# Performance work log

Hardware: AMD Instinct MI355X
Metric: run time of the kernel (lower is better)

## Reference

```python
import jax, jax.numpy as jnp
import numpy as np

B, S, D = 2, 1024, 2048
H, KV, HD = 16, 4, 128
GROUPS = H // KV
THETA = 10000.0


def act_quant(xr, xi):
    # per-token 8-bit absmax quantization over last dim, joint scale for re/im, STE
    amax = jnp.maximum(jnp.max(jnp.abs(xr), -1, keepdims=True),
                       jnp.max(jnp.abs(xi), -1, keepdims=True))
    s = 127.0 / jnp.maximum(amax, 1e-5)
    qr = jnp.clip(jnp.round(xr * s), -128, 127) / s
    qi = jnp.clip(jnp.round(xi * s), -128, 127) / s
    return xr + jax.lax.stop_gradient(qr - xr), xi + jax.lax.stop_gradient(qi - xi)


def weight_quant(wr, wi):
    # Fairy+-i direction quantization: each weight -> scale * d, d in {+1,-1,+i,-i}; STE
    mag = jnp.mean(jnp.sqrt(wr * wr + wi * wi))
    use_re = jnp.abs(wr) >= jnp.abs(wi)
    qr = jnp.where(use_re, jnp.sign(wr) * mag, 0.0)
    qi = jnp.where(use_re, 0.0, jnp.sign(wi) * mag)
    return wr + jax.lax.stop_gradient(qr - wr), wi + jax.lax.stop_gradient(qi - wi)


def complex_linear(xr, xi, wr, wi):
    xr, xi = act_quant(xr, xi)
    wr, wi = weight_quant(wr, wi)
    o_re = xr @ wr - xi @ wi
    o_im = xr @ wi + xi @ wr
    return o_re, o_im


def rotate_half(x):
    h = x.shape[-1] // 2
    return jnp.concatenate([-x[..., h:], x[..., :h]], axis=-1)


def rope_tables():
    inv_freq = 1.0 / (THETA ** (jnp.arange(0, HD, 2, dtype=jnp.float32) / HD))
    pos = jnp.arange(S, dtype=jnp.float32)
    freqs = pos[:, None] * inv_freq[None, :]          # [S, HD/2]
    emb = jnp.concatenate([freqs, freqs], axis=-1)    # [S, HD]
    return jnp.cos(emb)[None, None], jnp.sin(emb)[None, None]  # [1,1,S,HD]


def _heads(x, n):
    # [B,S,n*HD] -> [B,n,S,HD]
    return x.reshape(B, S, n, HD).transpose(0, 2, 1, 3)


def _attn(hidden_real, hidden_imag, wq_re, wq_im, wk_re, wk_im,
          wv_re, wv_im, wo_re, wo_im):
    q_re, q_im = complex_linear(hidden_real, hidden_imag, wq_re, wq_im)
    k_re, k_im = complex_linear(hidden_real, hidden_imag, wk_re, wk_im)
    v_re, v_im = complex_linear(hidden_real, hidden_imag, wv_re, wv_im)

    q_re, q_im = _heads(q_re, H), _heads(q_im, H)      # [B,H,S,HD]
    k_re, k_im = _heads(k_re, KV), _heads(k_im, KV)    # [B,KV,S,HD]
    v_re, v_im = _heads(v_re, KV), _heads(v_im, KV)

    cos, sin = rope_tables()
    # RoPE applied only to real components of q and k
    q_re = q_re * cos + rotate_half(q_re) * sin
    k_re = k_re * cos + rotate_half(k_re) * sin

    # GQA repeat
    k_re = jnp.repeat(k_re, GROUPS, axis=1)
    k_im = jnp.repeat(k_im, GROUPS, axis=1)
    v_re = jnp.repeat(v_re, GROUPS, axis=1)
    v_im = jnp.repeat(v_im, GROUPS, axis=1)

    # real scores = Re(q . conj(k)) = q_re.k_re + q_im.k_im
    scores = (jnp.einsum('bhqd,bhkd->bhqk', q_re, k_re) +
              jnp.einsum('bhqd,bhkd->bhqk', q_im, k_im)) / jnp.sqrt(jnp.float32(HD))
    causal = jnp.tril(jnp.ones((S, S), dtype=bool))
    scores = jnp.where(causal[None, None], scores, jnp.finfo(scores.dtype).min)
    attn = jax.nn.softmax(scores, axis=-1)

    o_re = jnp.einsum('bhqk,bhkd->bhqd', attn, v_re)
    o_im = jnp.einsum('bhqk,bhkd->bhqd', attn, v_im)
    o_re = o_re.transpose(0, 2, 1, 3).reshape(B, S, H * HD)
    o_im = o_im.transpose(0, 2, 1, 3).reshape(B, S, H * HD)

    out_re, out_im = complex_linear(o_re, o_im, wo_re, wo_im)
    return jnp.stack([out_re, out_im])  # [2,B,S,D]


def setup_inputs() -> dict:
    key = jax.random.key(0)
    ks = jax.random.split(key, 12)
    w = lambda k, shp: jax.random.normal(k, shp, dtype=jnp.float32) * 0.02
    return {
        'hidden_real': jax.random.normal(ks[0], (B, S, D), dtype=jnp.float32),
        'hidden_imag': jax.random.normal(ks[1], (B, S, D), dtype=jnp.float32),
        'wq_re': w(ks[2], (D, H * HD)), 'wq_im': w(ks[3], (D, H * HD)),
        'wk_re': w(ks[4], (D, KV * HD)), 'wk_im': w(ks[5], (D, KV * HD)),
        'wv_re': w(ks[6], (D, KV * HD)), 'wv_im': w(ks[7], (D, KV * HD)),
        'wo_re': w(ks[8], (H * HD, D)), 'wo_im': w(ks[9], (H * HD, D)),
    }


def reference(hidden_real, hidden_imag, wq_re, wq_im, wk_re, wk_im,
              wv_re, wv_im, wo_re, wo_im):
    return _attn(hidden_real, hidden_imag, wq_re, wq_im, wk_re, wk_im,
                 wv_re, wv_im, wo_re, wo_im)
```

## Files before the change

### kernel.cpp

```cpp
#include <hip/hip_runtime.h>
#include <stdint.h>

#define B_   2
#define S_   1024
#define D_   2048
#define H_   16
#define KV_  4
#define HD_  128
#define NTOK (B_ * S_)
#define QD   (H_ * HD_)
#define KD   (KV_ * HD_)

using i32x4  = __attribute__((ext_vector_type(4)))  int;
using i32x16 = __attribute__((ext_vector_type(16))) int;
using f32x4  = __attribute__((ext_vector_type(4)))  float;
using bf16x8 = __attribute__((ext_vector_type(8)))  short;

#define LN1E4_OVER_64 0.14391156831212725f

__device__ __forceinline__ float bf2f(uint16_t u) { return __uint_as_float((uint32_t)u << 16); }
__device__ __forceinline__ uint16_t f2bf(float f) {
    uint32_t u = __float_as_uint(f);
    return (uint16_t)((u + 0x7FFFu + ((u >> 16) & 1u)) >> 16);
}

__global__ __launch_bounds__(256)
void act_quant_i8_kernel(const float* __restrict__ xr, const float* __restrict__ xi,
                         int8_t* __restrict__ qr, int8_t* __restrict__ qi,
                         float* __restrict__ invs)
{
    const int tok = blockIdx.x, t = threadIdx.x;
    const float* pr = xr + (size_t)tok * 2048 + t * 8;
    const float* pi = xi + (size_t)tok * 2048 + t * 8;
    float4 r0 = *(const float4*)pr, r1 = *(const float4*)(pr + 4);
    float4 i0 = *(const float4*)pi, i1 = *(const float4*)(pi + 4);
    float am = fmaxf(fmaxf(fmaxf(fabsf(r0.x), fabsf(r0.y)), fmaxf(fabsf(r0.z), fabsf(r0.w))),
                     fmaxf(fmaxf(fabsf(r1.x), fabsf(r1.y)), fmaxf(fabsf(r1.z), fabsf(r1.w))));
    am = fmaxf(am, fmaxf(fmaxf(fmaxf(fabsf(i0.x), fabsf(i0.y)), fmaxf(fabsf(i0.z), fabsf(i0.w))),
                         fmaxf(fmaxf(fabsf(i1.x), fabsf(i1.y)), fmaxf(fabsf(i1.z), fabsf(i1.w)))));
    __shared__ float red[256];
    red[t] = am;
    __syncthreads();
    for (int st = 128; st > 0; st >>= 1) {
        if (t < st) red[t] = fmaxf(red[t], red[t + st]);
        __syncthreads();
    }
    const float s = 127.0f / fmaxf(red[0], 1e-5f);
    if (t == 0) invs[tok] = 1.0f / s;
#define Q8(x) ((uint32_t)(uint8_t)(int8_t)(int)fminf(fmaxf(rintf((x) * s), -128.f), 127.f))
    uint32_t a0 = Q8(r0.x) | (Q8(r0.y) << 8) | (Q8(r0.z) << 16) | (Q8(r0.w) << 24);
    uint32_t a1 = Q8(r1.x) | (Q8(r1.y) << 8) | (Q8(r1.z) << 16) | (Q8(r1.w) << 24);
    uint32_t b0 = Q8(i0.x) | (Q8(i0.y) << 8) | (Q8(i0.z) << 16) | (Q8(i0.w) << 24);
    uint32_t b1 = Q8(i1.x) | (Q8(i1.y) << 8) | (Q8(i1.z) << 16) | (Q8(i1.w) << 24);
#undef Q8
    *(uint32_t*)(qr + (size_t)tok * 2048 + t * 8)     = a0;
    *(uint32_t*)(qr + (size_t)tok * 2048 + t * 8 + 4) = a1;
    *(uint32_t*)(qi + (size_t)tok * 2048 + t * 8)     = b0;
    *(uint32_t*)(qi + (size_t)tok * 2048 + t * 8 + 4) = b1;
}

__global__ __launch_bounds__(256)
void decode_kernel(const float* __restrict__ wr, const float* __restrict__ wi,
                   int N, int8_t* __restrict__ psr, int8_t* __restrict__ psi,
                   int8_t* __restrict__ pnsi, int n_off, float* __restrict__ mag_out)
{
    __shared__ alignas(16) int8_t tr[3][64][80];
    __shared__ float red[256];
    const int n0 = blockIdx.x * 64, k0 = blockIdx.y * 64;
    float msum = 0.f;
    for (int idx = threadIdx.x; idx < 4096; idx += 256) {
        int j = idx & 63, i = idx >> 6;
        size_t g = (size_t)(k0 + i) * N + n0 + j;
        float a = wr[g], b = wi[g];
        msum += sqrtf(a * a + b * b);
        int8_t sr, si;
        if (fabsf(a) >= fabsf(b)) {
            sr = (a > 0.f) ? 1 : ((a < 0.f) ? -1 : 0);
            si = 0;
        } else {
            sr = 0;
            si = (b > 0.f) ? 1 : ((b < 0.f) ? -1 : 0);
        }
        tr[0][j][i] = sr;
        tr[1][j][i] = si;
        tr[2][j][i] = (int8_t)(-si);
    }
    red[threadIdx.x] = msum;
    __syncthreads();
    for (int st = 128; st > 0; st >>= 1) {
        if (threadIdx.x < st) red[threadIdx.x] += red[threadIdx.x + st];
        __syncthreads();
    }
    if (threadIdx.x == 0) atomicAdd(mag_out, red[0]);
    int8_t* planes[3] = { psr, psi, pnsi };
    for (int idx = threadIdx.x; idx < 768; idx += 256) {
        int p = idx >> 8, rem = idx & 255, n = rem >> 2, c = rem & 3;
        int4 v = *(const int4*)&tr[p][n][c * 16];
        *(int4*)(planes[p] + (size_t)(n_off + n0 + n) * 2048 + k0 + c * 16) = v;
    }
}

__device__ __forceinline__ void async_copy16(const void* g, void* l) {
    __builtin_amdgcn_global_load_lds((const __attribute__((address_space(1))) void*)g,
                                     (__attribute__((address_space(3))) void*)l, 16, 0, 0);
}

template <int MODE>
__global__ __launch_bounds__(256)
void gemm_i8_kernel(const int8_t* __restrict__ axr, const int8_t* __restrict__ axi,
                    const int8_t* __restrict__ bsr, const int8_t* __restrict__ bsi,
                    const int8_t* __restrict__ bnsi,
                    int Nout, const float* __restrict__ invs,
                    const float* __restrict__ mag_sums,
                    float magc0, float magc1, float magc2,
                    float* o_re, float* o_im,
                    uint16_t* kbr, uint16_t* kbi, uint16_t* vbr, uint16_t* vbi)
{
    __shared__ alignas(16) int8_t smem[2][5 * 8192];
    const int tid = threadIdx.x;
    const int wav = tid >> 6, lane = tid & 63;
    const int tileM = blockIdx.y * 128, tileN = blockIdx.x * 128;
    const int wm = wav & 1, wn = wav >> 1;
    const int K = 2048;

    const int8_t* gplane[5] = { axr, axi, bsr, bsi, bnsi };
    const int     rbase[5]  = { tileM, tileM, tileN, tileN, tileN };

    i32x16 acc_re[2][2] = {};
    i32x16 acc_im[2][2] = {};

    auto issue_tile = [&](int k0, int buf) {
#pragma unroll
        for (int i = 0; i < 10; ++i) {
            int q = wav + 4 * i;
            int pl = q >> 3, seg = q & 7;
            int c = seg >> 1, m0 = (seg & 1) << 6;
            const int8_t* g = gplane[pl] + (size_t)(rbase[pl] + m0 + lane) * K + k0 + c * 16;
            int8_t* l = &smem[buf][pl * 8192 + (c * 128 + m0) * 16];
            async_copy16(g, l);
        }
    };

    issue_tile(0, 0);
    issue_tile(64, 1);

    for (int k = 0; k < 32; ++k) {
        if (k == 31) { asm volatile("s_waitcnt vmcnt(0)" ::: "memory"); }
        else         { asm volatile("s_waitcnt vmcnt(10)" ::: "memory"); }
        asm volatile("s_barrier" ::: "memory");
        const int8_t* sb = smem[k & 1];
#pragma unroll
        for (int s = 0; s < 2; ++s) {
            const int cc = 2 * s + (lane >> 5);
            const int rA = wm * 64 + (lane & 31);
            const int rB = wn * 64 + (lane & 31);
            i32x4 fxr[2], fxi[2], fsr[2], fsi[2], fns[2];
#pragma unroll
            for (int mb = 0; mb < 2; ++mb) {
                int off = (cc * 128 + rA + mb * 32) * 16;
                fxr[mb] = *(const i32x4*)&sb[0 * 8192 + off];
                fxi[mb] = *(const i32x4*)&sb[1 * 8192 + off];
            }
#pragma unroll
            for (int nb = 0; nb < 2; ++nb) {
                int off = (cc * 128 + rB + nb * 32) * 16;
                fsr[nb] = *(const i32x4*)&sb[2 * 8192 + off];
                fsi[nb] = *(const i32x4*)&sb[3 * 8192 + off];
                fns[nb] = *(const i32x4*)&sb[4 * 8192 + off];
            }
#pragma unroll
            for (int mb = 0; mb < 2; ++mb)
#pragma unroll
                for (int nb = 0; nb < 2; ++nb) {
                    acc_re[mb][nb] = __builtin_amdgcn_mfma_i32_32x32x32_i8(fxr[mb], fsr[nb], acc_re[mb][nb], 0, 0, 0);
                    acc_re[mb][nb] = __builtin_amdgcn_mfma_i32_32x32x32_i8(fxi[mb], fns[nb], acc_re[mb][nb], 0, 0, 0);
                    acc_im[mb][nb] = __builtin_amdgcn_mfma_i32_32x32x32_i8(fxr[mb], fsi[nb], acc_im[mb][nb], 0, 0, 0);
                    acc_im[mb][nb] = __builtin_amdgcn_mfma_i32_32x32x32_i8(fxi[mb], fsr[nb], acc_im[mb][nb], 0, 0, 0);
                }
        }
        asm volatile("s_barrier" ::: "memory");
        if (k + 2 < 32) issue_tile((k + 2) * 64, k & 1);
    }

    const int ln31 = lane & 31, lq = lane >> 5;
#pragma unroll
    for (int mb = 0; mb < 2; ++mb) {
#pragma unroll
        for (int nb = 0; nb < 2; ++nb) {
            const int gn = tileN + wn * 64 + nb * 32 + ln31;
            float mag;
            if (MODE == 0)
                mag = (gn < 2048) ? mag_sums[0] * magc0
                    : (gn < 2560) ? mag_sums[1] * magc1
                                  : mag_sums[2] * magc2;
            else
                mag = mag_sums[0] * magc0;
#pragma unroll
            for (int r = 0; r < 16; ++r) {
                const int row = (r & 3) + 8 * (r >> 2) + 4 * lq;
                const int gm = tileM + wm * 64 + mb * 32 + row;
                const float sc = mag * invs[gm];
                const float re = (float)acc_re[mb][nb][r] * sc;
                const float im = (float)acc_im[mb][nb][r] * sc;
                if (MODE == 1) {
                    o_re[(size_t)gm * Nout + gn] = re;
                    o_im[(size_t)gm * Nout + gn] = im;
                } else {
                    const int s = gm & (S_ - 1), bb = gm >> 10;
                    if (gn < 2048) {
                        o_re[(size_t)gm * 2048 + gn] = re;
                        o_im[(size_t)gm * 2048 + gn] = im;
                    } else if (gn < 2560) {
                        int c = gn - 2048, kvh = c >> 7, d = c & 127;
                        size_t off = ((size_t)(bb * KV_ + kvh) * S_ + s) * 128 + d;
                        kbr[off] = f2bf(re);
                        kbi[off] = f2bf(im);
                    } else {
                        int c = gn - 2560, kvh = c >> 7, d = c & 127;
                        size_t off = ((size_t)(bb * KV_ + kvh) * S_ + s) * 128 + d;
                        vbr[off] = f2bf(re);
                        vbi[off] = f2bf(im);
                    }
                }
            }
        }
    }
}

__global__ __launch_bounds__(256)
void rope_q_kernel(const float* __restrict__ q_re, const float* __restrict__ q_im,
                   uint16_t* __restrict__ qb_re, uint16_t* __restrict__ qb_im)
{
    int gidx = blockIdx.x * 256 + threadIdx.x;
    int j = gidx & 15, h = (gidx >> 4) & 15, tok = gidx >> 8;
    int s = tok & (S_ - 1), b = tok >> 10;
    int d0 = j * 4;
    size_t ib = (size_t)tok * 2048 + h * 128;
    float4 r0 = *(const float4*)&q_re[ib + d0];
    float4 r1 = *(const float4*)&q_re[ib + d0 + 64];
    float4 i0 = *(const float4*)&q_im[ib + d0];
    float4 i1 = *(const float4*)&q_im[ib + d0 + 64];
    float ro0[4], ro1[4];
    float rv0[4] = { r0.x, r0.y, r0.z, r0.w };
    float rv1[4] = { r1.x, r1.y, r1.z, r1.w };
#pragma unroll
    for (int t = 0; t < 4; ++t) {
        float f = __expf(-(float)(d0 + t) * LN1E4_OVER_64);
        float sn, c;
        __sincosf((float)s * f, &sn, &c);
        ro0[t] = rv0[t] * c - rv1[t] * sn;
        ro1[t] = rv1[t] * c + rv0[t] * sn;
    }
    size_t ob = ((size_t)(b * H_ + h) * S_ + s) * 128;
    ushort4 w;
    w = (ushort4){ f2bf(ro0[0]), f2bf(ro0[1]), f2bf(ro0[2]), f2bf(ro0[3]) };
    *(ushort4*)&qb_re[ob + d0] = w;
    w = (ushort4){ f2bf(ro1[0]), f2bf(ro1[1]), f2bf(ro1[2]), f2bf(ro1[3]) };
    *(ushort4*)&qb_re[ob + d0 + 64] = w;
    w = (ushort4){ f2bf(i0.x), f2bf(i0.y), f2bf(i0.z), f2bf(i0.w) };
    *(ushort4*)&qb_im[ob + d0] = w;
    w = (ushort4){ f2bf(i1.x), f2bf(i1.y), f2bf(i1.z), f2bf(i1.w) };
    *(ushort4*)&qb_im[ob + d0 + 64] = w;
}

__global__ __launch_bounds__(256)
void rope_k_kernel(uint16_t* __restrict__ kb_re)
{
    int gidx = blockIdx.x * 256 + threadIdx.x;
    int j = gidx & 15, kvh = (gidx >> 4) & 3;
    int rest = gidx >> 6;
    int s = rest & (S_ - 1), b = rest >> 10;
    int d0 = j * 4;
    size_t base = ((size_t)(b * KV_ + kvh) * S_ + s) * 128;
    ushort4 u0 = *(const ushort4*)&kb_re[base + d0];
    ushort4 u1 = *(const ushort4*)&kb_re[base + d0 + 64];
    float rv0[4] = { bf2f(u0.x), bf2f(u0.y), bf2f(u0.z), bf2f(u0.w) };
    float rv1[4] = { bf2f(u1.x), bf2f(u1.y), bf2f(u1.z), bf2f(u1.w) };
    float ro0[4], ro1[4];
#pragma unroll
    for (int t = 0; t < 4; ++t) {
        float f = __expf(-(float)(d0 + t) * LN1E4_OVER_64);
        float sn, c;
        __sincosf((float)s * f, &sn, &c);
        ro0[t] = rv0[t] * c - rv1[t] * sn;
        ro1[t] = rv1[t] * c + rv0[t] * sn;
    }
    *(ushort4*)&kb_re[base + d0]      = (ushort4){ f2bf(ro0[0]), f2bf(ro0[1]), f2bf(ro0[2]), f2bf(ro0[3]) };
    *(ushort4*)&kb_re[base + d0 + 64] = (ushort4){ f2bf(ro1[0]), f2bf(ro1[1]), f2bf(ro1[2]), f2bf(ro1[3]) };
}

__global__ __launch_bounds__(256)
void vtrans_kernel(const uint16_t* __restrict__ vbr, const uint16_t* __restrict__ vbi,
                   uint16_t* __restrict__ vtr, uint16_t* __restrict__ vti)
{
    __shared__ uint16_t t[32][36];
    const int pl = blockIdx.z & 1, bk = blockIdx.z >> 1;
    const int s0 = blockIdx.x * 32, d0 = blockIdx.y * 32;
    const uint16_t* src = (pl ? vbi : vbr) + ((size_t)bk * S_) * 128;
    uint16_t*       dst = (pl ? vti : vtr) + ((size_t)bk * 128) * S_;
    const int r = threadIdx.x >> 3, c = (threadIdx.x & 7) * 4;
    *(ushort4*)&t[r][c] = *(const ushort4*)&src[(size_t)(s0 + r) * 128 + d0 + c];
    __syncthreads();
    ushort4 o = (ushort4){ t[c][r], t[c + 1][r], t[c + 2][r], t[c + 3][r] };
    *(ushort4*)&dst[(size_t)(d0 + r) * S_ + s0 + c] = o;
}

__global__ __launch_bounds__(256)
void attn_mfma_kernel(const uint16_t* __restrict__ qb_re, const uint16_t* __restrict__ qb_im,
                      const uint16_t* __restrict__ kb_re, const uint16_t* __restrict__ kb_im,
                      const uint16_t* __restrict__ vt_re, const uint16_t* __restrict__ vt_im,
                      float* __restrict__ o_re, float* __restrict__ o_im)
{
    __shared__ alignas(16) uint16_t sk[2][32][136];
    __shared__ alignas(16) uint16_t sv[2][128][40];
    __shared__ alignas(16) uint16_t sp[4][16][40];

    const int tid = threadIdx.x;
    const int w = tid >> 6, lane = tid & 63;
    const int r16 = lane & 15, q4 = lane >> 4;
    const int qt = gridDim.x - 1 - blockIdx.x;
    const int h = blockIdx.y, b = blockIdx.z;
    const int kvh = h >> 2;
    const int q0 = qt * 64, qw0 = q0 + w * 16;

    bf16x8 qfr[4], qfi[4];
    {
        const size_t qbase = ((size_t)(b * H_ + h) * S_ + qw0 + r16) * 128;
#pragma unroll
        for (int ks = 0; ks < 4; ++ks) {
            const int col = ks * 32 + q4 * 8;
            qfr[ks] = *(const bf16x8*)&qb_re[qbase + col];
            qfi[ks] = *(const bf16x8*)&qb_im[qbase + col];
        }
    }

    f32x4 oa[2][8] = {};
    float m_r[4] = { -3e38f, -3e38f, -3e38f, -3e38f };
    float l_r[4] = { 0.f, 0.f, 0.f, 0.f };

    const size_t kgbase0 = (size_t)(b * KV_ + kvh) * S_ * 128;
    const size_t vgbase0 = (size_t)(b * KV_ + kvh) * 128 * (size_t)S_;

    for (int c0 = 0; c0 < q0 + 64; c0 += 32) {
        for (int idx = tid; idx < 1024; idx += 256) {
            int pl = idx >> 9, c = idx & 511, r = c >> 4, ch = c & 15;
            const uint16_t* src = (pl ? kb_im : kb_re) + kgbase0 + (size_t)(c0 + r) * 128 + ch * 8;
            *(uint4*)&sk[pl][r][ch * 8] = *(const uint4*)src;
        }
        for (int idx = tid; idx < 1024; idx += 256) {
            int pl = idx >> 9, c = idx & 511, d = c >> 2, ch = c & 3;
            const uint16_t* src = (pl ? vt_im : vt_re) + vgbase0 + (size_t)d * S_ + c0 + ch * 8;
            *(uint4*)&sv[pl][d][ch * 8] = *(const uint4*)src;
        }
        __syncthreads();

        if (c0 <= qw0 + 15) {
            f32x4 sc[2] = {};
#pragma unroll
            for (int cblk = 0; cblk < 2; ++cblk) {
                const int krow = cblk * 16 + r16;
#pragma unroll
                for (int ks = 0; ks < 4; ++ks) {
                    const int kcol = ks * 32 + q4 * 8;
                    bf16x8 kr = *(const bf16x8*)&sk[0][krow][kcol];
                    bf16x8 ki = *(const bf16x8*)&sk[1][krow][kcol];
                    sc[cblk] = __builtin_amdgcn_mfma_f32_16x16x32_bf16(qfr[ks], kr, sc[cblk], 0, 0, 0);
                    sc[cblk] = __builtin_amdgcn_mfma_f32_16x16x32_bf16(qfi[ks], ki, sc[cblk], 0, 0, 0);
                }
            }
#pragma unroll
            for (int cblk = 0; cblk < 2; ++cblk)
#pragma unroll
                for (int reg = 0; reg < 4; ++reg) {
                    float sval = sc[cblk][reg] * 0.08838834764831845f;
                    const int rowg = qw0 + q4 * 4 + reg;
                    const int colg = c0 + cblk * 16 + r16;
                    if (colg > rowg) sval = -3e38f;
                    sc[cblk][reg] = sval;
                }
            float al[4];
#pragma unroll
            for (int reg = 0; reg < 4; ++reg) {
                float mx = fmaxf(sc[0][reg], sc[1][reg]);
#pragma unroll
                for (int msk = 1; msk < 16; msk <<= 1) mx = fmaxf(mx, __shfl_xor(mx, msk));
                const float mn = fmaxf(m_r[reg], mx);
                al[reg] = __expf(m_r[reg] - mn);
                const float p0 = __expf(sc[0][reg] - mn);
                const float p1 = __expf(sc[1][reg] - mn);
                sc[0][reg] = p0; sc[1][reg] = p1;
                float rs = p0 + p1;
#pragma unroll
                for (int msk = 1; msk < 16; msk <<= 1) rs += __shfl_xor(rs, msk);
                l_r[reg] = l_r[reg] * al[reg] + rs;
                m_r[reg] = mn;
            }
#pragma unroll
            for (int cblk = 0; cblk < 2; ++cblk)
#pragma unroll
                for (int reg = 0; reg < 4; ++reg)
                    sp[w][q4 * 4 + reg][cblk * 16 + r16] = f2bf(sc[cblk][reg]);
#pragma unroll
            for (int dblk = 0; dblk < 8; ++dblk)
#pragma unroll
                for (int reg = 0; reg < 4; ++reg) {
                    oa[0][dblk][reg] *= al[reg];
                    oa[1][dblk][reg] *= al[reg];
                }
            bf16x8 pf = *(const bf16x8*)&sp[w][r16][q4 * 8];
#pragma unroll
            for (int dblk = 0; dblk < 8; ++dblk) {
                const int vrow = dblk * 16 + r16;
                bf16x8 vr = *(const bf16x8*)&sv[0][vrow][q4 * 8];
                bf16x8 vi = *(const bf16x8*)&sv[1][vrow][q4 * 8];
                oa[0][dblk] = __builtin_amdgcn_mfma_f32_16x16x32_bf16(pf, vr, oa[0][dblk], 0, 0, 0);
                oa[1][dblk] = __builtin_amdgcn_mfma_f32_16x16x32_bf16(pf, vi, oa[1][dblk], 0, 0, 0);
            }
        }
        __syncthreads();
    }

    float inv[4];
#pragma unroll
    for (int reg = 0; reg < 4; ++reg) inv[reg] = 1.f / l_r[reg];
#pragma unroll
    for (int dblk = 0; dblk < 8; ++dblk) {
        const int col = h * 128 + dblk * 16 + r16;
#pragma unroll
        for (int reg = 0; reg < 4; ++reg) {
            const size_t tok = (size_t)b * S_ + qw0 + q4 * 4 + reg;
            o_re[tok * 2048 + col] = oa[0][dblk][reg] * inv[reg];
            o_im[tok * 2048 + col] = oa[1][dblk][reg] * inv[reg];
        }
    }
}

extern "C" void kernel_launch(void* const* d_in, const int* in_sizes, int n_in,
                              void* d_out, int out_size, void* d_ws, size_t ws_size,
                              hipStream_t stream)
{
    const float* hr    = (const float*)d_in[0];
    const float* hi    = (const float*)d_in[1];
    const float* wq_re = (const float*)d_in[2];
    const float* wq_im = (const float*)d_in[3];
    const float* wk_re = (const float*)d_in[4];
    const float* wk_im = (const float*)d_in[5];
    const float* wv_re = (const float*)d_in[6];
    const float* wv_im = (const float*)d_in[7];
    const float* wo_re = (const float*)d_in[8];
    const float* wo_im = (const float*)d_in[9];
    float* out = (float*)d_out;
    char*  base = (char*)d_ws;

    const size_t MB4  = (size_t)2048 * 2048;
    const size_t QKVP = (size_t)3072 * 2048;
    const size_t KVE  = (size_t)B_ * KV_ * S_ * 128;

    float*   mags   = (float*)(base);
    float*   invs1  = (float*)(base + 1024);
    float*   invs2  = (float*)(base + 9216);
    int8_t*  xr_q   = (int8_t*)(base + 32768);
    int8_t*  xi_q   = xr_q + MB4;
    int8_t*  qkv_sr = xi_q + MB4;
    int8_t*  qkv_si = qkv_sr + QKVP;
    int8_t*  qkv_ns = qkv_si + QKVP;
    int8_t*  wo_sr  = qkv_ns + QKVP;
    int8_t*  wo_si  = wo_sr + MB4;
    int8_t*  wo_ns  = wo_si + MB4;
    float*   q_re   = (float*)(wo_ns + MB4);
    float*   q_im   = q_re + MB4;
    uint16_t* kb_re = (uint16_t*)(q_im + MB4);
    uint16_t* kb_im = kb_re + KVE;
    uint16_t* vb_re = kb_im + KVE;
    uint16_t* vb_im = vb_re + KVE;
    uint16_t* vt_re = (uint16_t*)xr_q;
    uint16_t* vt_im = (uint16_t*)xi_q;
    uint16_t* qb_re = (uint16_t*)qkv_sr;
    uint16_t* qb_im = (uint16_t*)(qkv_sr + 8388608);

    hipMemsetAsync(mags, 0, 16, stream);

    decode_kernel<<<dim3(32, 32), 256, 0, stream>>>(wq_re, wq_im, 2048, qkv_sr, qkv_si, qkv_ns, 0,    mags + 0);
    decode_kernel<<<dim3(8, 32),  256, 0, stream>>>(wk_re, wk_im, 512,  qkv_sr, qkv_si, qkv_ns, 2048, mags + 1);
    decode_kernel<<<dim3(8, 32),  256, 0, stream>>>(wv_re, wv_im, 512,  qkv_sr, qkv_si, qkv_ns, 2560, mags + 2);
    decode_kernel<<<dim3(32, 32), 256, 0, stream>>>(wo_re, wo_im, 2048, wo_sr, wo_si, wo_ns, 0,       mags + 3);

    act_quant_i8_kernel<<<NTOK, 256, 0, stream>>>(hr, hi, xr_q, xi_q, invs1);

    gemm_i8_kernel<0><<<dim3(24, 16), 256, 0, stream>>>(
        xr_q, xi_q, qkv_sr, qkv_si, qkv_ns, 0, invs1, mags,
        1.0f / (float)((size_t)D_ * QD), 1.0f / (float)((size_t)D_ * KD), 1.0f / (float)((size_t)D_ * KD),
        q_re, q_im, kb_re, kb_im, vb_re, vb_im);

    rope_q_kernel<<<NTOK * H_ * 16 / 256, 256, 0, stream>>>(q_re, q_im, qb_re, qb_im);
    rope_k_kernel<<<NTOK * KV_ * 16 / 256, 256, 0, stream>>>(kb_re);
    vtrans_kernel<<<dim3(S_ / 32, 128 / 32, B_ * KV_ * 2), 256, 0, stream>>>(vb_re, vb_im, vt_re, vt_im);

    attn_mfma_kernel<<<dim3(S_ / 64, H_, B_), 256, 0, stream>>>(
        qb_re, qb_im, kb_re, kb_im, vt_re, vt_im, q_re, q_im);

    act_quant_i8_kernel<<<NTOK, 256, 0, stream>>>(q_re, q_im, xr_q, xi_q, invs2);

    gemm_i8_kernel<1><<<dim3(16, 16), 256, 0, stream>>>(
        xr_q, xi_q, wo_sr, wo_si, wo_ns, 2048, invs2, mags + 3,
        1.0f / (float)((size_t)QD * D_), 0.f, 0.f,
        out, out + MB4, nullptr, nullptr, nullptr, nullptr);
}
```

Measured before the change: 533.5 us.

## Fuse Q RoPE into attention, write V transposed from GEMM, drop LDS staging

```diff
diff --git a/kernel.cpp b/kernel.cpp
--- a/kernel.cpp
+++ b/kernel.cpp
@@ -114,12 +114,16 @@
                     const float* __restrict__ mag_sums,
                     float magc0, float magc1, float magc2,
                     float* o_re, float* o_im,
-                    uint16_t* kbr, uint16_t* kbi, uint16_t* vbr, uint16_t* vbi)
+                    uint16_t* kbr, uint16_t* kbi, uint16_t* vtr, uint16_t* vti)
 {
     __shared__ alignas(16) int8_t smem[2][5 * 8192];
     const int tid = threadIdx.x;
     const int wav = tid >> 6, lane = tid & 63;
-    const int tileM = blockIdx.y * 128, tileN = blockIdx.x * 128;
+    const int l = blockIdx.y * gridDim.x + blockIdx.x;
+    const int cpx = gridDim.x >> 3;
+    const int s7 = l >> 3;
+    const int tileN = ((l & 7) * cpx + (s7 >> 4)) * 128;
+    const int tileM = (s7 & 15) * 128;
     const int wm = wav & 1, wn = wav >> 1;
     const int K = 2048;
 
@@ -136,8 +140,8 @@
             int pl = q >> 3, seg = q & 7;
             int c = seg >> 1, m0 = (seg & 1) << 6;
             const int8_t* g = gplane[pl] + (size_t)(rbase[pl] + m0 + lane) * K + k0 + c * 16;
-            int8_t* l = &smem[buf][pl * 8192 + (c * 128 + m0) * 16];
-            async_copy16(g, l);
+            int8_t* lp = &smem[buf][pl * 8192 + (c * 128 + m0) * 16];
+            async_copy16(g, lp);
         }
     };
 
@@ -217,50 +221,14 @@
                         kbi[off] = f2bf(im);
                     } else {
                         int c = gn - 2560, kvh = c >> 7, d = c & 127;
-                        size_t off = ((size_t)(bb * KV_ + kvh) * S_ + s) * 128 + d;
-                        vbr[off] = f2bf(re);
-                        vbi[off] = f2bf(im);
+                        size_t off = ((size_t)(bb * KV_ + kvh) * 128 + d) * (size_t)S_ + s;
+                        vtr[off] = f2bf(re);
+                        vti[off] = f2bf(im);
                     }
                 }
             }
         }
     }
-}
-
-__global__ __launch_bounds__(256)
-void rope_q_kernel(const float* __restrict__ q_re, const float* __restrict__ q_im,
-                   uint16_t* __restrict__ qb_re, uint16_t* __restrict__ qb_im)
-{
-    int gidx = blockIdx.x * 256 + threadIdx.x;
-    int j = gidx & 15, h = (gidx >> 4) & 15, tok = gidx >> 8;
-    int s = tok & (S_ - 1), b = tok >> 10;
-    int d0 = j * 4;
-    size_t ib = (size_t)tok * 2048 + h * 128;
-    float4 r0 = *(const float4*)&q_re[ib + d0];
-    float4 r1 = *(const float4*)&q_re[ib + d0 + 64];
-    float4 i0 = *(const float4*)&q_im[ib + d0];
-    float4 i1 = *(const float4*)&q_im[ib + d0 + 64];
-    float ro0[4], ro1[4];
-    float rv0[4] = { r0.x, r0.y, r0.z, r0.w };
-    float rv1[4] = { r1.x, r1.y, r1.z, r1.w };
-#pragma unroll
-    for (int t = 0; t < 4; ++t) {
-        float f = __expf(-(float)(d0 + t) * LN1E4_OVER_64);
-        float sn, c;
-        __sincosf((float)s * f, &sn, &c);
-        ro0[t] = rv0[t] * c - rv1[t] * sn;
-        ro1[t] = rv1[t] * c + rv0[t] * sn;
-    }
-    size_t ob = ((size_t)(b * H_ + h) * S_ + s) * 128;
-    ushort4 w;
-    w = (ushort4){ f2bf(ro0[0]), f2bf(ro0[1]), f2bf(ro0[2]), f2bf(ro0[3]) };
-    *(ushort4*)&qb_re[ob + d0] = w;
-    w = (ushort4){ f2bf(ro1[0]), f2bf(ro1[1]), f2bf(ro1[2]), f2bf(ro1[3]) };
-    *(ushort4*)&qb_re[ob + d0 + 64] = w;
-    w = (ushort4){ f2bf(i0.x), f2bf(i0.y), f2bf(i0.z), f2bf(i0.w) };
-    *(ushort4*)&qb_im[ob + d0] = w;
-    w = (ushort4){ f2bf(i1.x), f2bf(i1.y), f2bf(i1.z), f2bf(i1.w) };
-    *(ushort4*)&qb_im[ob + d0 + 64] = w;
 }
 
 __global__ __launch_bounds__(256)
@@ -290,29 +258,11 @@
 }
 
 __global__ __launch_bounds__(256)
-void vtrans_kernel(const uint16_t* __restrict__ vbr, const uint16_t* __restrict__ vbi,
-                   uint16_t* __restrict__ vtr, uint16_t* __restrict__ vti)
-{
-    __shared__ uint16_t t[32][36];
-    const int pl = blockIdx.z & 1, bk = blockIdx.z >> 1;
-    const int s0 = blockIdx.x * 32, d0 = blockIdx.y * 32;
-    const uint16_t* src = (pl ? vbi : vbr) + ((size_t)bk * S_) * 128;
-    uint16_t*       dst = (pl ? vti : vtr) + ((size_t)bk * 128) * S_;
-    const int r = threadIdx.x >> 3, c = (threadIdx.x & 7) * 4;
-    *(ushort4*)&t[r][c] = *(const ushort4*)&src[(size_t)(s0 + r) * 128 + d0 + c];
-    __syncthreads();
-    ushort4 o = (ushort4){ t[c][r], t[c + 1][r], t[c + 2][r], t[c + 3][r] };
-    *(ushort4*)&dst[(size_t)(d0 + r) * S_ + s0 + c] = o;
-}
-
-__global__ __launch_bounds__(256)
-void attn_mfma_kernel(const uint16_t* __restrict__ qb_re, const uint16_t* __restrict__ qb_im,
+void attn_mfma_kernel(const float* __restrict__ q_re, const float* __restrict__ q_im,
                       const uint16_t* __restrict__ kb_re, const uint16_t* __restrict__ kb_im,
                       const uint16_t* __restrict__ vt_re, const uint16_t* __restrict__ vt_im,
                       float* __restrict__ o_re, float* __restrict__ o_im)
 {
-    __shared__ alignas(16) uint16_t sk[2][32][136];
-    __shared__ alignas(16) uint16_t sv[2][128][40];
     __shared__ alignas(16) uint16_t sp[4][16][40];
 
     const int tid = threadIdx.x;
@@ -321,103 +271,114 @@
     const int qt = gridDim.x - 1 - blockIdx.x;
     const int h = blockIdx.y, b = blockIdx.z;
     const int kvh = h >> 2;
-    const int q0 = qt * 64, qw0 = q0 + w * 16;
+    const int qw0 = qt * 64 + w * 16;
+    const int srow = qw0 + r16;
 
     bf16x8 qfr[4], qfi[4];
     {
-        const size_t qbase = ((size_t)(b * H_ + h) * S_ + qw0 + r16) * 128;
+        const size_t qbase = ((size_t)(b * S_ + srow)) * 2048 + h * 128;
+        float fre[4][8];
 #pragma unroll
         for (int ks = 0; ks < 4; ++ks) {
             const int col = ks * 32 + q4 * 8;
-            qfr[ks] = *(const bf16x8*)&qb_re[qbase + col];
-            qfi[ks] = *(const bf16x8*)&qb_im[qbase + col];
-        }
+            float4 a = *(const float4*)&q_re[qbase + col];
+            float4 bb4 = *(const float4*)&q_re[qbase + col + 4];
+            fre[ks][0] = a.x; fre[ks][1] = a.y; fre[ks][2] = a.z; fre[ks][3] = a.w;
+            fre[ks][4] = bb4.x; fre[ks][5] = bb4.y; fre[ks][6] = bb4.z; fre[ks][7] = bb4.w;
+            float4 c4 = *(const float4*)&q_im[qbase + col];
+            float4 d4 = *(const float4*)&q_im[qbase + col + 4];
+            qfi[ks][0] = (short)f2bf(c4.x); qfi[ks][1] = (short)f2bf(c4.y);
+            qfi[ks][2] = (short)f2bf(c4.z); qfi[ks][3] = (short)f2bf(c4.w);
+            qfi[ks][4] = (short)f2bf(d4.x); qfi[ks][5] = (short)f2bf(d4.y);
+            qfi[ks][6] = (short)f2bf(d4.z); qfi[ks][7] = (short)f2bf(d4.w);
+        }
+#pragma unroll
+        for (int kp = 0; kp < 2; ++kp)
+#pragma unroll
+            for (int j = 0; j < 8; ++j) {
+                const int d = kp * 32 + q4 * 8 + j;
+                float f = __expf(-(float)d * LN1E4_OVER_64);
+                float sn, cc;
+                __sincosf((float)srow * f, &sn, &cc);
+                float v0 = fre[kp][j], v1 = fre[kp + 2][j];
+                fre[kp][j]     = v0 * cc - v1 * sn;
+                fre[kp + 2][j] = v1 * cc + v0 * sn;
+            }
+#pragma unroll
+        for (int ks = 0; ks < 4; ++ks)
+#pragma unroll
+            for (int j = 0; j < 8; ++j)
+                qfr[ks][j] = (short)f2bf(fre[ks][j]);
     }
 
     f32x4 oa[2][8] = {};
     float m_r[4] = { -3e38f, -3e38f, -3e38f, -3e38f };
     float l_r[4] = { 0.f, 0.f, 0.f, 0.f };
 
-    const size_t kgbase0 = (size_t)(b * KV_ + kvh) * S_ * 128;
-    const size_t vgbase0 = (size_t)(b * KV_ + kvh) * 128 * (size_t)S_;
-
-    for (int c0 = 0; c0 < q0 + 64; c0 += 32) {
-        for (int idx = tid; idx < 1024; idx += 256) {
-            int pl = idx >> 9, c = idx & 511, r = c >> 4, ch = c & 15;
-            const uint16_t* src = (pl ? kb_im : kb_re) + kgbase0 + (size_t)(c0 + r) * 128 + ch * 8;
-            *(uint4*)&sk[pl][r][ch * 8] = *(const uint4*)src;
-        }
-        for (int idx = tid; idx < 1024; idx += 256) {
-            int pl = idx >> 9, c = idx & 511, d = c >> 2, ch = c & 3;
-            const uint16_t* src = (pl ? vt_im : vt_re) + vgbase0 + (size_t)d * S_ + c0 + ch * 8;
-            *(uint4*)&sv[pl][d][ch * 8] = *(const uint4*)src;
-        }
-        __syncthreads();
-
-        if (c0 <= qw0 + 15) {
-            f32x4 sc[2] = {};
-#pragma unroll
-            for (int cblk = 0; cblk < 2; ++cblk) {
-                const int krow = cblk * 16 + r16;
-#pragma unroll
-                for (int ks = 0; ks < 4; ++ks) {
-                    const int kcol = ks * 32 + q4 * 8;
-                    bf16x8 kr = *(const bf16x8*)&sk[0][krow][kcol];
-                    bf16x8 ki = *(const bf16x8*)&sk[1][krow][kcol];
-                    sc[cblk] = __builtin_amdgcn_mfma_f32_16x16x32_bf16(qfr[ks], kr, sc[cblk], 0, 0, 0);
-                    sc[cblk] = __builtin_amdgcn_mfma_f32_16x16x32_bf16(qfi[ks], ki, sc[cblk], 0, 0, 0);
-                }
-            }
-#pragma unroll
-            for (int cblk = 0; cblk < 2; ++cblk)
-#pragma unroll
-                for (int reg = 0; reg < 4; ++reg) {
-                    float sval = sc[cblk][reg] * 0.08838834764831845f;
-                    const int rowg = qw0 + q4 * 4 + reg;
-                    const int colg = c0 + cblk * 16 + r16;
-                    if (colg > rowg) sval = -3e38f;
-                    sc[cblk][reg] = sval;
-                }
-            float al[4];
+    const size_t kgbase = (size_t)(b * KV_ + kvh) * S_ * 128;
+    const size_t vgbase = (size_t)(b * KV_ + kvh) * 128 * (size_t)S_;
+
+    for (int c0 = 0; c0 < qw0 + 16; c0 += 32) {
+        f32x4 sc[2] = {};
+#pragma unroll
+        for (int cblk = 0; cblk < 2; ++cblk) {
+            const size_t krow = kgbase + (size_t)(c0 + cblk * 16 + r16) * 128 + q4 * 8;
+#pragma unroll
+            for (int ks = 0; ks < 4; ++ks) {
+                bf16x8 kr = *(const bf16x8*)&kb_re[krow + ks * 32];
+                bf16x8 ki = *(const bf16x8*)&kb_im[krow + ks * 32];
+                sc[cblk] = __builtin_amdgcn_mfma_f32_16x16x32_bf16(qfr[ks], kr, sc[cblk], 0, 0, 0);
+                sc[cblk] = __builtin_amdgcn_mfma_f32_16x16x32_bf16(qfi[ks], ki, sc[cblk], 0, 0, 0);
+            }
+        }
+#pragma unroll
+        for (int cblk = 0; cblk < 2; ++cblk)
 #pragma unroll
             for (int reg = 0; reg < 4; ++reg) {
-                float mx = fmaxf(sc[0][reg], sc[1][reg]);
-#pragma unroll
-                for (int msk = 1; msk < 16; msk <<= 1) mx = fmaxf(mx, __shfl_xor(mx, msk));
-                const float mn = fmaxf(m_r[reg], mx);
-                al[reg] = __expf(m_r[reg] - mn);
-                const float p0 = __expf(sc[0][reg] - mn);
-                const float p1 = __expf(sc[1][reg] - mn);
-                sc[0][reg] = p0; sc[1][reg] = p1;
-                float rs = p0 + p1;
-#pragma unroll
-                for (int msk = 1; msk < 16; msk <<= 1) rs += __shfl_xor(rs, msk);
-                l_r[reg] = l_r[reg] * al[reg] + rs;
-                m_r[reg] = mn;
-            }
-#pragma unroll
-            for (int cblk = 0; cblk < 2; ++cblk)
-#pragma unroll
-                for (int reg = 0; reg < 4; ++reg)
-                    sp[w][q4 * 4 + reg][cblk * 16 + r16] = f2bf(sc[cblk][reg]);
-#pragma unroll
-            for (int dblk = 0; dblk < 8; ++dblk)
-#pragma unroll
-                for (int reg = 0; reg < 4; ++reg) {
-                    oa[0][dblk][reg] *= al[reg];
-                    oa[1][dblk][reg] *= al[reg];
-                }
-            bf16x8 pf = *(const bf16x8*)&sp[w][r16][q4 * 8];
-#pragma unroll
-            for (int dblk = 0; dblk < 8; ++dblk) {
-                const int vrow = dblk * 16 + r16;
-                bf16x8 vr = *(const bf16x8*)&sv[0][vrow][q4 * 8];
-                bf16x8 vi = *(const bf16x8*)&sv[1][vrow][q4 * 8];
-                oa[0][dblk] = __builtin_amdgcn_mfma_f32_16x16x32_bf16(pf, vr, oa[0][dblk], 0, 0, 0);
-                oa[1][dblk] = __builtin_amdgcn_mfma_f32_16x16x32_bf16(pf, vi, oa[1][dblk], 0, 0, 0);
-            }
-        }
-        __syncthreads();
+                float sval = sc[cblk][reg] * 0.08838834764831845f;
+                const int rowg = qw0 + q4 * 4 + reg;
+                const int colg = c0 + cblk * 16 + r16;
+                if (colg > rowg) sval = -3e38f;
+                sc[cblk][reg] = sval;
+            }
+        float al[4];
+#pragma unroll
+        for (int reg = 0; reg < 4; ++reg) {
+            float mx = fmaxf(sc[0][reg], sc[1][reg]);
+#pragma unroll
+            for (int msk = 1; msk < 16; msk <<= 1) mx = fmaxf(mx, __shfl_xor(mx, msk));
+            const float mn = fmaxf(m_r[reg], mx);
+            al[reg] = __expf(m_r[reg] - mn);
+            const float p0 = __expf(sc[0][reg] - mn);
+            const float p1 = __expf(sc[1][reg] - mn);
+            sc[0][reg] = p0; sc[1][reg] = p1;
+            float rs = p0 + p1;
+#pragma unroll
+            for (int msk = 1; msk < 16; msk <<= 1) rs += __shfl_xor(rs, msk);
+            l_r[reg] = l_r[reg] * al[reg] + rs;
+            m_r[reg] = mn;
+        }
+#pragma unroll
+        for (int cblk = 0; cblk < 2; ++cblk)
+#pragma unroll
+            for (int reg = 0; reg < 4; ++reg)
+                sp[w][q4 * 4 + reg][cblk * 16 + r16] = f2bf(sc[cblk][reg]);
+#pragma unroll
+        for (int dblk = 0; dblk < 8; ++dblk)
+#pragma unroll
+            for (int reg = 0; reg < 4; ++reg) {
+                oa[0][dblk][reg] *= al[reg];
+                oa[1][dblk][reg] *= al[reg];
+            }
+        bf16x8 pf = *(const bf16x8*)&sp[w][r16][q4 * 8];
+#pragma unroll
+        for (int dblk = 0; dblk < 8; ++dblk) {
+            const size_t vrow = vgbase + (size_t)(dblk * 16 + r16) * S_ + c0 + q4 * 8;
+            bf16x8 vr = *(const bf16x8*)&vt_re[vrow];
+            bf16x8 vi = *(const bf16x8*)&vt_im[vrow];
+            oa[0][dblk] = __builtin_amdgcn_mfma_f32_16x16x32_bf16(pf, vr, oa[0][dblk], 0, 0, 0);
+            oa[1][dblk] = __builtin_amdgcn_mfma_f32_16x16x32_bf16(pf, vi, oa[1][dblk], 0, 0, 0);
+        }
     }
 
     float inv[4];
@@ -471,12 +432,8 @@
     float*   q_im   = q_re + MB4;
     uint16_t* kb_re = (uint16_t*)(q_im + MB4);
     uint16_t* kb_im = kb_re + KVE;
-    uint16_t* vb_re = kb_im + KVE;
-    uint16_t* vb_im = vb_re + KVE;
-    uint16_t* vt_re = (uint16_t*)xr_q;
-    uint16_t* vt_im = (uint16_t*)xi_q;
-    uint16_t* qb_re = (uint16_t*)qkv_sr;
-    uint16_t* qb_im = (uint16_t*)(qkv_sr + 8388608);
+    uint16_t* vt_re = kb_im + KVE;
+    uint16_t* vt_im = vt_re + KVE;
 
     hipMemsetAsync(mags, 0, 16, stream);
 
@@ -490,14 +447,12 @@
     gemm_i8_kernel<0><<<dim3(24, 16), 256, 0, stream>>>(
         xr_q, xi_q, qkv_sr, qkv_si, qkv_ns, 0, invs1, mags,
         1.0f / (float)((size_t)D_ * QD), 1.0f / (float)((size_t)D_ * KD), 1.0f / (float)((size_t)D_ * KD),
-        q_re, q_im, kb_re, kb_im, vb_re, vb_im);
-
-    rope_q_kernel<<<NTOK * H_ * 16 / 256, 256, 0, stream>>>(q_re, q_im, qb_re, qb_im);
+        q_re, q_im, kb_re, kb_im, vt_re, vt_im);
+
     rope_k_kernel<<<NTOK * KV_ * 16 / 256, 256, 0, stream>>>(kb_re);
-    vtrans_kernel<<<dim3(S_ / 32, 128 / 32, B_ * KV_ * 2), 256, 0, stream>>>(vb_re, vb_im, vt_re, vt_im);
 
     attn_mfma_kernel<<<dim3(S_ / 64, H_, B_), 256, 0, stream>>>(
-        qb_re, qb_im, kb_re, kb_im, vt_re, vt_im, q_re, q_im);
+        q_re, q_im, kb_re, kb_im, vt_re, vt_im, q_re, q_im);
 
     act_quant_i8_kernel<<<NTOK, 256, 0, stream>>>(q_re, q_im, xr_q, xi_q, invs2);
 
```

After: 642.0 us. 20.3% more time.
